# Optimization experiments

Hardware: AMD Instinct MI355X
Metric: run time of the kernel (lower is better)

The kernel has to match this reference:

```python
import jax, jax.numpy as jnp
import numpy as np

N_NODES = 100000
N_EDGES = 1600000
F_IN = 256
DIM = 32
N_CLASSES = 40


def setup_inputs() -> dict:
    key = jax.random.key(0)
    ks = jax.random.split(key, 8)
    x = jax.random.normal(ks[0], (N_NODES, F_IN), dtype=jnp.float32)
    edge_index = jax.random.randint(ks[1], (2, N_EDGES), 0, N_NODES, dtype=jnp.int64)
    s1 = 1.0 / np.sqrt(F_IN)
    s2 = 1.0 / np.sqrt(DIM)
    return {
        "x": x,
        "edge_index": edge_index,
        # SAGEConv layer 1: lin_l (aggregated neighbors, with bias) + lin_r (root)
        "W1l": jax.random.uniform(ks[2], (F_IN, DIM), jnp.float32, -s1, s1),
        "W1r": jax.random.uniform(ks[3], (F_IN, DIM), jnp.float32, -s1, s1),
        "b1": jnp.zeros((DIM,), jnp.float32),
        # SAGEConv layer 2
        "W2l": jax.random.uniform(ks[4], (DIM, N_CLASSES), jnp.float32, -s2, s2),
        "W2r": jax.random.uniform(ks[5], (DIM, N_CLASSES), jnp.float32, -s2, s2),
        "b2": jnp.zeros((N_CLASSES,), jnp.float32),
    }


def reference(x, edge_index, W1l, W1r, b1, W2l, W2r, b2):
    N = x.shape[0]
    src, dst = edge_index[0], edge_index[1]
    # in-degree for mean aggregation (clamped to avoid div-by-zero, matching
    # PyG mean-scatter semantics where isolated nodes get zeros)
    deg = jax.ops.segment_sum(jnp.ones_like(src, dtype=x.dtype), dst, num_segments=N)
    inv_deg = (1.0 / jnp.maximum(deg, 1.0))[:, None]  # [N,1]

    def sage_conv(h, Wl, Wr, b):
        # mean over incoming neighbor features, then linear + root linear
        agg = jax.ops.segment_sum(h[src], dst, num_segments=N) * inv_deg  # [N,F]
        return agg @ Wl + h @ Wr + b

    h = jax.nn.relu(sage_conv(x, W1l, W1r, b1))
    # F.dropout(p=0.5, training=self.training): identity in eval mode
    h = sage_conv(h, W2l, W2r, b2)
    return jax.nn.log_softmax(h, axis=1)
```

## Files before the change

### kernel.cpp

```cpp
#include <hip/hip_runtime.h>
#include <hip/hip_bf16.h>
#include <math.h>

#define N_NODES 100000
#define N_EDGES 1600000
#define F_IN 256
#define DIM 32
#define NC 40
#define NCP 48

#define NBLK 391

#define NPART 8
#define FPART_SZ 12500

typedef _Float16 half_t;
typedef _Float16 h8 __attribute__((ext_vector_type(8)));
typedef float f32x4 __attribute__((ext_vector_type(4)));
union H8 { float4 f4; half_t h[8]; };

__global__ void deg_kernel(const int* __restrict__ dst, int* __restrict__ degi) {
    int i = blockIdx.x * blockDim.x + threadIdx.x;
    if (i < N_EDGES) atomicAdd(&degi[dst[i]], 1);
}

__device__ __forceinline__ int block_scan_excl(int v, int& tot) {
    int lane = threadIdx.x & 63;
    int wid = threadIdx.x >> 6;
    int s = v;
#pragma unroll
    for (int off = 1; off < 64; off <<= 1) {
        int t = __shfl_up(s, off, 64);
        if (lane >= off) s += t;
    }
    __shared__ int wsum[8];
    if (lane == 63) wsum[wid] = s;
    __syncthreads();
    int nw = (blockDim.x + 63) >> 6;
    int wprev = 0, total = 0;
    for (int i = 0; i < nw; ++i) {
        int t = wsum[i];
        if (i < wid) wprev += t;
        total += t;
    }
    tot = total;
    return wprev + s - v;
}

__global__ void scanA_kernel(const int* __restrict__ degi, int* __restrict__ partial) {
    int i = blockIdx.x * 256 + threadIdx.x;
    int v = (i < N_NODES) ? degi[i] : 0;
    int tot;
    block_scan_excl(v, tot);
    if (threadIdx.x == 0) partial[blockIdx.x] = tot;
}

__global__ void scanB_kernel(int* __restrict__ partial, int* __restrict__ blockoff) {
    int i = threadIdx.x;
    int v = (i < NBLK) ? partial[i] : 0;
    int tot;
    int ex = block_scan_excl(v, tot);
    if (i < NBLK) blockoff[i] = ex;
}

__global__ void scanC_kernel(const int* __restrict__ degi,
                             const int* __restrict__ blockoff,
                             int* __restrict__ rowstart,
                             int* __restrict__ cursor) {
    int i = blockIdx.x * 256 + threadIdx.x;
    int v = (i < N_NODES) ? degi[i] : 0;
    int tot;
    int ex = block_scan_excl(v, tot) + blockoff[blockIdx.x];
    if (i < N_NODES) {
        rowstart[i] = ex;
        cursor[i] = ex;
    }
}

__global__ __launch_bounds__(256)
void fill_xcd_kernel(const int* __restrict__ src,
                     const int* __restrict__ dst,
                     int* __restrict__ cursor,
                     int* __restrict__ csr) {
    int x = blockIdx.x & (NPART - 1);
    int gblk = blockIdx.x >> 3;
    int gsize = gridDim.x >> 3;
    int tid = gblk * blockDim.x + threadIdx.x;
    int stride = gsize * blockDim.x;
    int lo = x * FPART_SZ;
    int hi = (x == NPART - 1) ? N_NODES : lo + FPART_SZ;

    const int4* dst4 = (const int4*)dst;
    for (int e4 = tid; e4 < N_EDGES / 4; e4 += stride) {
        int4 d4 = dst4[e4];
        int e = e4 * 4;
#pragma unroll
        for (int c = 0; c < 4; ++c) {
            int d = (c == 0) ? d4.x : (c == 1) ? d4.y : (c == 2) ? d4.z : d4.w;
            if (d >= lo && d < hi) {
                int pos = atomicAdd(&cursor[d], 1);
                csr[pos] = src[e + c];
            }
        }
    }
}

__global__ void wconv1(const float* __restrict__ W1l,
                       const float* __restrict__ W1r,
                       half_t* __restrict__ Wt) {
    int i = blockIdx.x * 256 + threadIdx.x;
    if (i >= 64 * F_IN) return;
    int c = i >> 8;
    int k = i & 255;
    float v = (c < DIM) ? W1l[(size_t)k * DIM + c] : W1r[(size_t)k * DIM + (c - DIM)];
    Wt[i] = (half_t)v;
}

__global__ void wconv2(const float* __restrict__ W2l,
                       const float* __restrict__ W2r,
                       half_t* __restrict__ Wt2l,
                       half_t* __restrict__ Wt2r) {
    int i = blockIdx.x * 256 + threadIdx.x;
    if (i >= 2 * NCP * DIM) return;
    int tab = i >= NCP * DIM;
    int j = i - tab * NCP * DIM;
    int c = j >> 5;
    int k = j & 31;
    const float* W = tab ? W2r : W2l;
    half_t* T = tab ? Wt2r : Wt2l;
    float v = (c < NC) ? W[(size_t)k * NC + c] : 0.f;
    T[j] = (half_t)v;
}

__global__ __launch_bounds__(256)
void proj1_mfma(const float* __restrict__ x,
                const half_t* __restrict__ Wt,
                half_t* __restrict__ P1h,
                half_t* __restrict__ R1h) {
    int wid = threadIdx.x >> 6;
    int lane = threadIdx.x & 63;
    int n0 = blockIdx.x * 64 + wid * 16;

    int arow = lane & 15;
    int kb = lane >> 4;
    int node = n0 + arow;
    int ldnode = node < N_NODES ? node : N_NODES - 1;
    const float* xrow = x + (size_t)ldnode * F_IN + kb * 8;
    const half_t* wb = Wt + (size_t)arow * F_IN + kb * 8;

    f32x4 acc[4];
#pragma unroll
    for (int ct = 0; ct < 4; ++ct) acc[ct] = (f32x4){0.f, 0.f, 0.f, 0.f};

#pragma unroll
    for (int k0 = 0; k0 < F_IN; k0 += 32) {
        float4 a0 = *(const float4*)&xrow[k0];
        float4 a1 = *(const float4*)&xrow[k0 + 4];
        h8 af;
        af[0] = (half_t)a0.x; af[1] = (half_t)a0.y;
        af[2] = (half_t)a0.z; af[3] = (half_t)a0.w;
        af[4] = (half_t)a1.x; af[5] = (half_t)a1.y;
        af[6] = (half_t)a1.z; af[7] = (half_t)a1.w;
#pragma unroll
        for (int ct = 0; ct < 4; ++ct) {
            h8 bf = *(const h8*)&wb[(size_t)ct * 16 * F_IN + k0];
            acc[ct] = __builtin_amdgcn_mfma_f32_16x16x32_f16(af, bf, acc[ct], 0, 0, 0);
        }
    }

    int jrow = (lane >> 4) * 4;
    int cc = lane & 15;
#pragma unroll
    for (int ct = 0; ct < 4; ++ct) {
        int cglob = ct * 16 + cc;
        half_t* outp = (cglob < DIM) ? (P1h + cglob) : (R1h + (cglob - DIM));
#pragma unroll
        for (int j = 0; j < 4; ++j) {
            int n = n0 + jrow + j;
            if (n < N_NODES) outp[(size_t)n * DIM] = (half_t)acc[ct][j];
        }
    }
}

__device__ __forceinline__ void gather_node(const int* __restrict__ csr,
                                            const half_t* __restrict__ feat,
                                            int rs, int re, int q8, float acc[8]) {
#pragma unroll
    for (int i = 0; i < 8; ++i) acc[i] = 0.f;
    int e = rs;
    for (; e + 2 <= re; e += 2) {
        int s0 = csr[e];
        int s1 = csr[e + 1];
        H8 u0, u1;
        u0.f4 = *(const float4*)&feat[(size_t)s0 * DIM + q8];
        u1.f4 = *(const float4*)&feat[(size_t)s1 * DIM + q8];
#pragma unroll
        for (int i = 0; i < 8; ++i) acc[i] += (float)u0.h[i] + (float)u1.h[i];
    }
    if (e < re) {
        int s0 = csr[e];
        H8 u0;
        u0.f4 = *(const float4*)&feat[(size_t)s0 * DIM + q8];
#pragma unroll
        for (int i = 0; i < 8; ++i) acc[i] += (float)u0.h[i];
    }
}

__global__ __launch_bounds__(256)
void agg1_h_kernel(const int* __restrict__ rowstart,
                   const int* __restrict__ degi,
                   const int* __restrict__ csr,
                   const half_t* __restrict__ P1h,
                   const half_t* __restrict__ R1h,
                   const float* __restrict__ b1,
                   half_t* __restrict__ h) {
    int wave = blockIdx.x * 4 + (threadIdx.x >> 6);
    int lane = threadIdx.x & 63;
    int node = wave * 16 + (lane >> 2);
    if (node >= N_NODES) return;
    int q8 = (lane & 3) * 8;
    int rs = rowstart[node];
    int dg = degi[node];
    float acc[8];
    gather_node(csr, P1h, rs, rs + dg, q8, acc);
    float inv = 1.0f / (float)max(dg, 1);
    H8 r;
    r.f4 = *(const float4*)&R1h[(size_t)node * DIM + q8];
    float4 bb0 = *(const float4*)&b1[q8];
    float4 bb1 = *(const float4*)&b1[q8 + 4];
    float rb[8] = { (float)r.h[0] + bb0.x, (float)r.h[1] + bb0.y,
                    (float)r.h[2] + bb0.z, (float)r.h[3] + bb0.w,
                    (float)r.h[4] + bb1.x, (float)r.h[5] + bb1.y,
                    (float)r.h[6] + bb1.z, (float)r.h[7] + bb1.w };
    H8 o;
#pragma unroll
    for (int i = 0; i < 8; ++i) {
        float v = fmaf(acc[i], inv, rb[i]);
        o.h[i] = (half_t)(v > 0.f ? v : 0.f);
    }
    *(float4*)&h[(size_t)node * DIM + q8] = o.f4;
}

__global__ __launch_bounds__(256)
void agg2_kernel(const int* __restrict__ rowstart,
                 const int* __restrict__ degi,
                 const int* __restrict__ csr,
                 const half_t* __restrict__ h,
                 half_t* __restrict__ a2h) {
    int wave = blockIdx.x * 4 + (threadIdx.x >> 6);
    int lane = threadIdx.x & 63;
    int node = wave * 16 + (lane >> 2);
    if (node >= N_NODES) return;
    int q8 = (lane & 3) * 8;
    int rs = rowstart[node];
    int dg = degi[node];
    float acc[8];
    gather_node(csr, h, rs, rs + dg, q8, acc);
    float inv = 1.0f / (float)max(dg, 1);
    H8 o;
#pragma unroll
    for (int i = 0; i < 8; ++i) o.h[i] = (half_t)(acc[i] * inv);
    *(float4*)&a2h[(size_t)node * DIM + q8] = o.f4;
}

__global__ __launch_bounds__(256)
void out_mfma(const half_t* __restrict__ a2h,
              const half_t* __restrict__ h,
              const half_t* __restrict__ Wt2l,
              const half_t* __restrict__ Wt2r,
              const float* __restrict__ b2,
              float* __restrict__ out) {
    int wid = threadIdx.x >> 6;
    int lane = threadIdx.x & 63;
    int n0 = blockIdx.x * 64 + wid * 16;
    if (n0 >= N_NODES) return;

    int arow = lane & 15;
    int kb = lane >> 4;
    int node = n0 + arow;
    int ldnode = node < N_NODES ? node : N_NODES - 1;

    h8 afA = *(const h8*)&a2h[(size_t)ldnode * DIM + kb * 8];
    h8 afH = *(const h8*)&h[(size_t)ldnode * DIM + kb * 8];

    f32x4 acc[3];
#pragma unroll
    for (int ct = 0; ct < 3; ++ct) {
        const h8 bl = *(const h8*)&Wt2l[(size_t)(ct * 16 + arow) * DIM + kb * 8];
        const h8 br = *(const h8*)&Wt2r[(size_t)(ct * 16 + arow) * DIM + kb * 8];
        f32x4 a = (f32x4){0.f, 0.f, 0.f, 0.f};
        a = __builtin_amdgcn_mfma_f32_16x16x32_f16(afA, bl, a, 0, 0, 0);
        a = __builtin_amdgcn_mfma_f32_16x16x32_f16(afH, br, a, 0, 0, 0);
        acc[ct] = a;
    }

    int cc = lane & 15;
#pragma unroll
    for (int ct = 0; ct < 3; ++ct) {
        int cglob = ct * 16 + cc;
        float bias = (cglob < NC) ? b2[cglob] : -1e30f;
#pragma unroll
        for (int j = 0; j < 4; ++j)
            acc[ct][j] = (cglob < NC) ? acc[ct][j] + bias : -1e30f;
    }

    float lg[4];
#pragma unroll
    for (int j = 0; j < 4; ++j) {
        float m = fmaxf(fmaxf(acc[0][j], acc[1][j]), acc[2][j]);
#pragma unroll
        for (int mk = 1; mk < 16; mk <<= 1)
            m = fmaxf(m, __shfl_xor(m, mk, 64));
        float s = __expf(acc[0][j] - m) + __expf(acc[1][j] - m) + __expf(acc[2][j] - m);
#pragma unroll
        for (int mk = 1; mk < 16; mk <<= 1)
            s += __shfl_xor(s, mk, 64);
        lg[j] = m + __logf(s);
    }

    int jrow = (lane >> 4) * 4;
#pragma unroll
    for (int ct = 0; ct < 3; ++ct) {
        int cglob = ct * 16 + cc;
        if (cglob < NC) {
#pragma unroll
            for (int j = 0; j < 4; ++j) {
                int n = n0 + jrow + j;
                if (n < N_NODES) out[(size_t)n * NC + cglob] = acc[ct][j] - lg[j];
            }
        }
    }
}

extern "C" void kernel_launch(void* const* d_in, const int* in_sizes, int n_in,
                              void* d_out, int out_size, void* d_ws, size_t ws_size,
                              hipStream_t stream) {
    const float* x   = (const float*)d_in[0];
    const int*   ei  = (const int*)d_in[1];
    const float* W1l = (const float*)d_in[2];
    const float* W1r = (const float*)d_in[3];
    const float* b1  = (const float*)d_in[4];
    const float* W2l = (const float*)d_in[5];
    const float* W2r = (const float*)d_in[6];
    const float* b2  = (const float*)d_in[7];
    float* out = (float*)d_out;

    const int* src = ei;
    const int* dst = ei + N_EDGES;

    char* ws = (char*)d_ws;
    int*    degi     = (int*)ws;      ws += sizeof(int) * 102400;
    int*    rowstart = (int*)ws;      ws += sizeof(int) * 102400;
    int*    cursor   = (int*)ws;      ws += sizeof(int) * 102400;
    int*    partial  = (int*)ws;      ws += sizeof(int) * 512;
    int*    blockoff = (int*)ws;      ws += sizeof(int) * 512;
    int*    csr      = (int*)ws;      ws += sizeof(int) * N_EDGES;
    half_t* P1h      = (half_t*)ws;   ws += sizeof(half_t) * N_NODES * DIM;
    half_t* h        = (half_t*)ws;   ws += sizeof(half_t) * N_NODES * DIM;
    half_t* a2h      = (half_t*)ws;   ws += sizeof(half_t) * N_NODES * DIM;
    half_t* R1h      = (half_t*)ws;   ws += sizeof(half_t) * N_NODES * DIM;
    half_t* Wt       = (half_t*)ws;   ws += sizeof(half_t) * 64 * F_IN;
    half_t* Wt2l     = (half_t*)ws;   ws += sizeof(half_t) * NCP * DIM;
    half_t* Wt2r     = (half_t*)ws;   ws += sizeof(half_t) * NCP * DIM;

    hipMemsetAsync(degi, 0, sizeof(int) * 102400, stream);

    wconv1<<<64, 256, 0, stream>>>(W1l, W1r, Wt);
    wconv2<<<12, 256, 0, stream>>>(W2l, W2r, Wt2l, Wt2r);
    deg_kernel<<<(N_EDGES + 255) / 256, 256, 0, stream>>>(dst, degi);
    scanA_kernel<<<NBLK, 256, 0, stream>>>(degi, partial);
    scanB_kernel<<<1, 512, 0, stream>>>(partial, blockoff);
    scanC_kernel<<<NBLK, 256, 0, stream>>>(degi, blockoff, rowstart, cursor);
    fill_xcd_kernel<<<2048, 256, 0, stream>>>(src, dst, cursor, csr);

    proj1_mfma<<<(N_NODES + 63) / 64, 256, 0, stream>>>(x, Wt, P1h, R1h);

    int gather_blocks = (N_NODES + 63) / 64;
    agg1_h_kernel<<<gather_blocks, 256, 0, stream>>>(rowstart, degi, csr, P1h, R1h, b1, h);
    agg2_kernel<<<gather_blocks, 256, 0, stream>>>(rowstart, degi, csr, h, a2h);
    out_mfma<<<(N_NODES + 63) / 64, 256, 0, stream>>>(a2h, h, Wt2l, Wt2r, b2, out);
}
```

Before: 388.2 us.

## Fuse CSR fill and layer-1 projection into one interleaved kernel

Merges the atomic CSR fill kernel and the MFMA input-projection kernel into a single launch whose blocks alternate between the two jobs in groups of 16. The latency-bound atomic scatter and the bandwidth-heavy read of x can then share the GPU concurrently instead of running back to back, and one launch boundary is removed. The fill keeps its XCD-partitioned block-to-partition mapping through blockIdx & 7, which the interleaving still preserves. The risk is that both halves compete for memory bandwidth, and the padded grid launches some idle blocks.

```diff
diff --git a/kernel.cpp b/kernel.cpp
--- a/kernel.cpp
+++ b/kernel.cpp
@@ -13,6 +13,9 @@
 
 #define NPART 8
 #define FPART_SZ 12500
+#define FILL_BLOCKS 2048
+#define PROJ_BLOCKS 1563
+#define FAT_GRID 4096
 
 typedef _Float16 half_t;
 typedef _Float16 h8 __attribute__((ext_vector_type(8)));
@@ -74,34 +77,6 @@
     if (i < N_NODES) {
         rowstart[i] = ex;
         cursor[i] = ex;
-    }
-}
-
-__global__ __launch_bounds__(256)
-void fill_xcd_kernel(const int* __restrict__ src,
-                     const int* __restrict__ dst,
-                     int* __restrict__ cursor,
-                     int* __restrict__ csr) {
-    int x = blockIdx.x & (NPART - 1);
-    int gblk = blockIdx.x >> 3;
-    int gsize = gridDim.x >> 3;
-    int tid = gblk * blockDim.x + threadIdx.x;
-    int stride = gsize * blockDim.x;
-    int lo = x * FPART_SZ;
-    int hi = (x == NPART - 1) ? N_NODES : lo + FPART_SZ;
-
-    const int4* dst4 = (const int4*)dst;
-    for (int e4 = tid; e4 < N_EDGES / 4; e4 += stride) {
-        int4 d4 = dst4[e4];
-        int e = e4 * 4;
-#pragma unroll
-        for (int c = 0; c < 4; ++c) {
-            int d = (c == 0) ? d4.x : (c == 1) ? d4.y : (c == 2) ? d4.z : d4.w;
-            if (d >= lo && d < hi) {
-                int pos = atomicAdd(&cursor[d], 1);
-                csr[pos] = src[e + c];
-            }
-        }
     }
 }
 
@@ -132,14 +107,41 @@
     T[j] = (half_t)v;
 }
 
-__global__ __launch_bounds__(256)
-void proj1_mfma(const float* __restrict__ x,
-                const half_t* __restrict__ Wt,
-                half_t* __restrict__ P1h,
-                half_t* __restrict__ R1h) {
+__device__ __forceinline__ void fill_body(int fid,
+                                          const int* __restrict__ src,
+                                          const int* __restrict__ dst,
+                                          int* __restrict__ cursor,
+                                          int* __restrict__ csr) {
+    int x = fid & (NPART - 1);
+    int gblk = fid >> 3;
+    int tid = gblk * 256 + threadIdx.x;
+    int stride = (FILL_BLOCKS >> 3) * 256;
+    int lo = x * FPART_SZ;
+    int hi = (x == NPART - 1) ? N_NODES : lo + FPART_SZ;
+
+    const int4* dst4 = (const int4*)dst;
+    for (int e4 = tid; e4 < N_EDGES / 4; e4 += stride) {
+        int4 d4 = dst4[e4];
+        int e = e4 * 4;
+#pragma unroll
+        for (int c = 0; c < 4; ++c) {
+            int d = (c == 0) ? d4.x : (c == 1) ? d4.y : (c == 2) ? d4.z : d4.w;
+            if (d >= lo && d < hi) {
+                int pos = atomicAdd(&cursor[d], 1);
+                csr[pos] = src[e + c];
+            }
+        }
+    }
+}
+
+__device__ __forceinline__ void proj_body(int pid,
+                                          const float* __restrict__ x,
+                                          const half_t* __restrict__ Wt,
+                                          half_t* __restrict__ P1h,
+                                          half_t* __restrict__ R1h) {
     int wid = threadIdx.x >> 6;
     int lane = threadIdx.x & 63;
-    int n0 = blockIdx.x * 64 + wid * 16;
+    int n0 = pid * 64 + wid * 16;
 
     int arow = lane & 15;
     int kb = lane >> 4;
@@ -179,6 +181,26 @@
             int n = n0 + jrow + j;
             if (n < N_NODES) outp[(size_t)n * DIM] = (half_t)acc[ct][j];
         }
+    }
+}
+
+__global__ __launch_bounds__(256)
+void fill_proj_kernel(const int* __restrict__ src,
+                      const int* __restrict__ dst,
+                      int* __restrict__ cursor,
+                      int* __restrict__ csr,
+                      const float* __restrict__ x,
+                      const half_t* __restrict__ Wt,
+                      half_t* __restrict__ P1h,
+                      half_t* __restrict__ R1h) {
+    int chunk = blockIdx.x >> 5;
+    int r = blockIdx.x & 31;
+    if (r < 16) {
+        int fid = chunk * 16 + r;
+        if (fid < FILL_BLOCKS) fill_body(fid, src, dst, cursor, csr);
+    } else {
+        int pid = chunk * 16 + (r - 16);
+        if (pid < PROJ_BLOCKS) proj_body(pid, x, Wt, P1h, R1h);
     }
 }
 
@@ -371,9 +393,9 @@
     scanA_kernel<<<NBLK, 256, 0, stream>>>(degi, partial);
     scanB_kernel<<<1, 512, 0, stream>>>(partial, blockoff);
     scanC_kernel<<<NBLK, 256, 0, stream>>>(degi, blockoff, rowstart, cursor);
-    fill_xcd_kernel<<<2048, 256, 0, stream>>>(src, dst, cursor, csr);
-
-    proj1_mfma<<<(N_NODES + 63) / 64, 256, 0, stream>>>(x, Wt, P1h, R1h);
+
+    fill_proj_kernel<<<FAT_GRID, 256, 0, stream>>>(src, dst, cursor, csr,
+                                                   x, Wt, P1h, R1h);
 
     int gather_blocks = (N_NODES + 63) / 64;
     agg1_h_kernel<<<gather_blocks, 256, 0, stream>>>(rowstart, degi, csr, P1h, R1h, b1, h);
```

Result: faster. 372.4 us (-4.1%).
